# Kernel optimization log

Hardware: AMD Instinct MI355X
Metric: run time of the kernel (lower is better)

Reference implementation:

```python
import jax, jax.numpy as jnp
import numpy as np

N, E, H = 50000, 500000, 4
DIN, DH, DO, TD = 135, 128, 64, 9

def _ln(x, g, b):
    mu = jnp.mean(x, axis=-1, keepdims=True)
    v = jnp.var(x, axis=-1, keepdims=True)
    return (x - mu) / jnp.sqrt(v + 1e-5) * g + b

def _gat(x, src, dst, W, a_src, a_dst, b, n, heads, c):
    h = (x @ W).reshape(n, heads, c)                      # [N,H,C]
    es = jnp.sum(h * a_src, -1)                           # [N,H]
    ed = jnp.sum(h * a_dst, -1)
    e = jax.nn.leaky_relu(es[src] + ed[dst], 0.2)         # [E,H]
    m = jax.ops.segment_max(e, dst, num_segments=n)       # segment softmax over dst
    ex = jnp.exp(e - m[dst])
    den = jax.ops.segment_sum(ex, dst, num_segments=n)
    alpha = ex / (den[dst] + 1e-16)
    out = jax.ops.segment_sum(h[src] * alpha[..., None], dst, num_segments=n)
    return jnp.mean(out, axis=1) + b                      # concat=False -> head mean

def setup_inputs() -> dict:
    key = jax.random.key(0)
    ks = jax.random.split(key, 32)
    rn = lambda i, shape: jax.random.normal(ks[i], shape, jnp.float32) * 0.05
    inp = {}
    inp['x'] = jax.random.normal(ks[0], (N, DIN), jnp.float32)
    inp['edge_index'] = jax.random.randint(ks[1], (2, E), 0, N, jnp.int32)
    inp['edge_attr'] = jnp.ones((E, 1), jnp.float32)
    inp['W_in'] = rn(2, (DIN, DH)); inp['b_in'] = jnp.zeros((DH,), jnp.float32)
    inp['g1W'] = rn(3, (DH, H * DH)); inp['g1as'] = rn(4, (H, DH)); inp['g1ad'] = rn(5, (H, DH)); inp['g1b'] = jnp.zeros((DH,), jnp.float32)
    inp['g2W'] = rn(6, (DH, H * DH)); inp['g2as'] = rn(7, (H, DH)); inp['g2ad'] = rn(8, (H, DH)); inp['g2b'] = jnp.zeros((DH,), jnp.float32)
    inp['g3W'] = rn(9, (DH, H * DO)); inp['g3as'] = rn(10, (H, DO)); inp['g3ad'] = rn(11, (H, DO)); inp['g3b'] = jnp.zeros((DO,), jnp.float32)
    inp['r1W'] = rn(12, (DH, DH)); inp['r1b'] = jnp.zeros((DH,), jnp.float32)
    inp['r2W'] = rn(13, (DH, DH)); inp['r2b'] = jnp.zeros((DH,), jnp.float32)
    inp['r3W'] = rn(14, (DH, DO)); inp['r3b'] = jnp.zeros((DO,), jnp.float32)
    inp['n1g'] = jnp.ones((DH,), jnp.float32); inp['n1b'] = jnp.zeros((DH,), jnp.float32)
    inp['n2g'] = jnp.ones((DH,), jnp.float32); inp['n2b'] = jnp.zeros((DH,), jnp.float32)
    inp['n3g'] = jnp.ones((DO,), jnp.float32); inp['n3b'] = jnp.zeros((DO,), jnp.float32)
    inp['tw'] = jnp.float32(0.3)
    inp['c1W'] = rn(15, (DO, DO)); inp['c1b'] = jnp.zeros((DO,), jnp.float32)
    inp['clg'] = jnp.ones((DO,), jnp.float32); inp['clb'] = jnp.zeros((DO,), jnp.float32)
    inp['c2W'] = rn(16, (DO, 2)); inp['c2b'] = jnp.zeros((2,), jnp.float32)
    return inp

def reference(x, edge_index, edge_attr, W_in, b_in, g1W, g1as, g1ad, g1b,
              g2W, g2as, g2ad, g2b, g3W, g3as, g3ad, g3b,
              r1W, r1b, r2W, r2b, r3W, r3b,
              n1g, n1b, n2g, n2b, n3g, n3b, tw,
              c1W, c1b, clg, clb, c2W, c2b):
    n = x.shape[0]
    src0, dst0 = edge_index[0], edge_index[1]
    loop = jnp.arange(n, dtype=edge_index.dtype)          # GATConv add_self_loops=True
    src = jnp.concatenate([src0, loop])
    dst = jnp.concatenate([dst0, loop])
    # vectorized temporal cosine similarity over original edges
    t = x[:, -TD:]
    ti, tj = t[src0], t[dst0]
    nrm = jnp.maximum(jnp.linalg.norm(ti, axis=-1), 1e-8) * jnp.maximum(jnp.linalg.norm(tj, axis=-1), 1e-8)
    sim = jnp.sum(ti * tj, -1) / nrm
    scale = 1.0 + 0.1 * jnp.mean(1.0 + tw * sim)
    h = x @ W_in + b_in
    id1 = h
    h = _gat(h, src, dst, g1W, g1as, g1ad, g1b, n, H, DH) * scale
    h = _ln(jax.nn.relu(h) + id1 @ r1W + r1b, n1g, n1b)
    id2 = h
    h = _gat(h, src, dst, g2W, g2as, g2ad, g2b, n, H, DH) * scale
    h = _ln(jax.nn.relu(h) + id2 @ r2W + r2b, n2g, n2b)
    id3 = h
    h = _gat(h, src, dst, g3W, g3as, g3ad, g3b, n, H, DO)
    h = _ln(jax.nn.relu(h) + id3 @ r3W + r3b, n3g, n3b)
    ego = h[0:1]
    z = jax.nn.relu(ego @ c1W + c1b)
    z = _ln(z, clg, clb)
    return z @ c2W + c2b
```

## Files before the change

kernel.cpp:

```cpp
#include <hip/hip_runtime.h>

#define AGENT __HIP_MEMORY_SCOPE_AGENT

constexpr int TD = 9, TDP = 12, DIN = 135;
constexpr int CAPD = 64;
constexpr int CAP3 = 256, CAP2 = 1024, CAP1 = 4096;
constexpr int NBM = 512;
constexpr int LSTRIDE = 32;
constexpr int NGRP = 16;
constexpr int GSZ = NBM / NGRP;
constexpr int NSET = 8;
constexpr int NLINE = 64;
constexpr int PB = 8;

struct P {
  const float* x; const int* src; const int* dst; int N; int E;
  const float *W_in,*b_in,*g1W,*g1as,*g1ad,*g1b,*g2W,*g2as,*g2ad,*g2b,*g3W,*g3as,*g3ad,*g3b;
  const float *r1W,*r1b,*r2W,*r2b,*r3W,*r3b,*n1g,*n1b,*n2g,*n2b,*n3g,*n3b;
  const float *tw,*c1W,*c1b,*clg,*clb,*c2W,*c2b;
  float* tp;
  int *deg, *bk;
  int *m3,*m2,*m1,*list3,*list2,*list1,*cnts;
  int *barc,*barr,*barg;
  float *h0,*hh1,*es1,*ed1,*h1,*hh2,*es2,*ed2,*h2,*hh3,*es3,*ed3,*h3;
  float* dout;
};

__device__ __forceinline__ float lrelu(float v) { return v >= 0.f ? v : 0.2f * v; }

__device__ __forceinline__ void stg(float* pp, float v) { __hip_atomic_store(pp, v, __ATOMIC_RELAXED, AGENT); }
__device__ __forceinline__ void stg(int* pp, int v)   { __hip_atomic_store(pp, v, __ATOMIC_RELAXED, AGENT); }

__device__ __forceinline__ void claim_node(int v, int* __restrict__ m, int* __restrict__ list,
                                           int* __restrict__ cnt, int cap) {
  if (atomicCAS(&m[v], -1, -2) == -1) {
    int pos = atomicAdd(cnt, 1);
    if (pos < cap) { stg(&list[pos], v); stg(&m[v], pos); } else { stg(&m[v], -3); }
  }
}

__device__ __forceinline__ void mid_barrier(const P& p, int& lgen, int* amroot_s) {
  __syncthreads();
  int g = lgen + 1;
  if (threadIdx.x == 0) {
    *amroot_s = 0;
    int* gc = &p.barc[(((g & (NSET - 1)) * NGRP) + (blockIdx.x & (NGRP - 1))) * LSTRIDE];
    if (__hip_atomic_fetch_add(gc, 1, __ATOMIC_RELAXED, AGENT) == GSZ - 1) {
      int* rc = &p.barr[(g & (NSET - 1)) * LSTRIDE];
      if (__hip_atomic_fetch_add(rc, 1, __ATOMIC_RELAXED, AGENT) == NGRP - 1) *amroot_s = 1;
    }
  }
  __syncthreads();
  if (*amroot_s) {
    if (threadIdx.x < NLINE)
      __hip_atomic_store(&p.barg[threadIdx.x * LSTRIDE], g, __ATOMIC_RELAXED, AGENT);
  } else if (threadIdx.x == 0) {
    int* line = &p.barg[(blockIdx.x & (NLINE - 1)) * LSTRIDE];
    while (__hip_atomic_load(line, __ATOMIC_RELAXED, AGENT) < g)
      __builtin_amdgcn_s_sleep(8);
  }
  __syncthreads();
  lgen = g;
}

__global__ void k_prep(P p) {
  int gt = blockIdx.x * blockDim.x + threadIdx.x;
  int GT = gridDim.x * blockDim.x;
  int n3 = 3 * p.N;
  int4* mv = (int4*)p.m3;
  int4 neg = make_int4(-1, -1, -1, -1);
  int nv = n3 >> 2;
  for (int i = gt; i < nv; i += GT) mv[i] = neg;
  for (int i = (nv << 2) + gt; i < n3; i += GT) p.m3[i] = -1;
  int4* dv = (int4*)p.deg;
  int4 z4 = make_int4(0, 0, 0, 0);
  int ndv = p.N >> 2;
  for (int i = gt; i < ndv; i += GT) dv[i] = z4;
  for (int i = (ndv << 2) + gt; i < p.N; i += GT) p.deg[i] = 0;
  if (gt < 64) p.cnts[gt] = 0;
  for (int i = gt; i < NSET * NGRP * LSTRIDE; i += GT) p.barc[i] = 0;
  for (int i = gt; i < NSET * LSTRIDE; i += GT) p.barr[i] = 0;
  for (int i = gt; i < NLINE * LSTRIDE; i += GT) p.barg[i] = 0;
  int total = p.N * TDP;
  for (int i = gt; i < total; i += GT) {
    int v = i / TDP, k = i - v * TDP;
    p.tp[i] = (k < TD) ? p.x[(size_t)v * DIN + (DIN - TD) + k] : 0.f;
  }
}

__global__ void k_scan(P p) {
  __shared__ float wred[4];
  int tid = threadIdx.x;
  int gt = blockIdx.x * blockDim.x + tid, GT = gridDim.x * blockDim.x;
  if (gt == 0) claim_node(0, p.m3, p.list3, &p.cnts[0], CAP3);
  const float4* t4 = (const float4*)p.tp;
  float local = 0.f;
  auto edge_proc = [&](int s, int d) {
    int slot = atomicAdd(&p.deg[d], 1);
    if (slot < CAPD) p.bk[(size_t)d * CAPD + slot] = s;
    if (d == 0) claim_node(s, p.m3, p.list3, &p.cnts[0], CAP3);
    float4 a0 = t4[s * 3], a1 = t4[s * 3 + 1], a2 = t4[s * 3 + 2];
    float4 b0 = t4[d * 3], b1 = t4[d * 3 + 1], b2 = t4[d * 3 + 2];
    float dot = a0.x*b0.x + a0.y*b0.y + a0.z*b0.z + a0.w*b0.w
              + a1.x*b1.x + a1.y*b1.y + a1.z*b1.z + a1.w*b1.w
              + a2.x*b2.x;
    float na = a0.x*a0.x + a0.y*a0.y + a0.z*a0.z + a0.w*a0.w
             + a1.x*a1.x + a1.y*a1.y + a1.z*a1.z + a1.w*a1.w
             + a2.x*a2.x;
    float nb = b0.x*b0.x + b0.y*b0.y + b0.z*b0.z + b0.w*b0.w
             + b1.x*b1.x + b1.y*b1.y + b1.z*b1.z + b1.w*b1.w
             + b2.x*b2.x;
    local += dot / (fmaxf(sqrtf(na), 1e-8f) * fmaxf(sqrtf(nb), 1e-8f));
  };
  int nq4 = p.E >> 2;
  const int4* s4p = (const int4*)p.src;
  const int4* d4p = (const int4*)p.dst;
  for (int q = gt; q < nq4; q += GT) {
    int4 s4 = s4p[q], d4 = d4p[q];
    edge_proc(s4.x, d4.x); edge_proc(s4.y, d4.y); edge_proc(s4.z, d4.z); edge_proc(s4.w, d4.w);
  }
  for (int e = (nq4 << 2) + gt; e < p.E; e += GT) edge_proc(p.src[e], p.dst[e]);
  for (int off = 32; off > 0; off >>= 1) local += __shfl_down(local, off, 64);
  if ((tid & 63) == 0) wred[tid >> 6] = local;
  __syncthreads();
  if (tid == 0) atomicAdd((float*)&p.cnts[8], wred[0] + wred[1] + wred[2] + wred[3]);
}

template <int C, int ONEXT>
__device__ void gat_dev(const P& p, int nq, const int* lst, const int* mPrev,
                        const float* hh, const float* es, const float* ed, const float* hres,
                        const float* gb, const float* rW, const float* rb,
                        const float* ng, const float* nbv, float scale,
                        float* hout, const float* Wn, const float* avn, const float* bvn,
                        float* hhn, float* esn, float* edn,
                        float* elog, int* eposs, float* ev_s, float* sh,
                        float* hres_s, float* shln, float* psn, float* pdn, float* sc2) {
  const int Wd = 4 * C, R = Wd / 256;
  int tid = threadIdx.x;
  for (int q = blockIdx.x; q < nq; q += gridDim.x) {
    int v = lst[q];
    int sp = mPrev[v];
    int nb = min(p.deg[v], CAPD);
    for (int j = tid; j < nb; j += 256) {
      int pu = mPrev[p.bk[(size_t)v * CAPD + j]];
      eposs[j] = pu;
      const float* ep = &es[(size_t)pu * 4];
      elog[0 * CAPD + j] = ep[0]; elog[1 * CAPD + j] = ep[1];
      elog[2 * CAPD + j] = ep[2]; elog[3 * CAPD + j] = ep[3];
    }
    if (tid < 4) { ev_s[tid] = es[(size_t)sp * 4 + tid]; ev_s[4 + tid] = ed[(size_t)sp * 4 + tid]; }
    for (int k = tid; k < 128; k += 256) hres_s[k] = hres[(size_t)sp * 128 + k];
    __syncthreads();
#pragma unroll
    for (int r = 0; r < R; r++) {
      int w = r * 256 + tid, a = w / C;
      float edv = ev_s[4 + a];
      float eself = lrelu(ev_s[a] + edv);
      float mx = eself;
      for (int j = 0; j < nb; j++) mx = fmaxf(mx, lrelu(elog[a * CAPD + j] + edv));
      float den = __expf(eself - mx);
      for (int j = 0; j < nb; j++) den += __expf(lrelu(elog[a * CAPD + j] + edv) - mx);
      float rden = 1.f / (den + 1e-16f);
      float s = __expf(eself - mx) * rden * hh[(size_t)sp * Wd + w];
      for (int j = 0; j < nb; j++)
        s += __expf(lrelu(elog[a * CAPD + j] + edv) - mx) * rden * hh[(size_t)eposs[j] * Wd + w];
      sh[w] = s;
    }
    __syncthreads();
    float val = 0.f;
    if (tid < C) {
      float g = 0.25f * (sh[tid] + sh[C + tid] + sh[2 * C + tid] + sh[3 * C + tid]) + gb[tid];
      g *= scale;
      g = fmaxf(g, 0.f);
      float rr = rb[tid];
      for (int k = 0; k < 128; k++) rr += hres_s[k] * rW[(size_t)k * C + tid];
      val = g + rr;
      shln[tid] = val;
    }
    __syncthreads();
    if (tid == 0) {
      float s1 = 0.f, s2 = 0.f;
      for (int k = 0; k < C; k++) { float u = shln[k]; s1 += u; s2 += u * u; }
      float mu = s1 / (float)C;
      sc2[0] = mu;
      sc2[1] = rsqrtf(fmaxf(s2 / (float)C - mu * mu, 0.f) + 1e-5f);
    }
    __syncthreads();
    if (tid < C) {
      float o = (val - sc2[0]) * sc2[1] * ng[tid] + nbv[tid];
      stg(&hout[(size_t)q * C + tid], o);
      shln[tid] = o;
    }
    __syncthreads();
    if (ONEXT > 0) {
      for (int j = tid; j < ONEXT; j += 256) {
        float a2 = 0.f;
        for (int k = 0; k < C; k++) a2 += shln[k] * Wn[(size_t)k * ONEXT + j];
        stg(&hhn[(size_t)q * ONEXT + j], a2);
        psn[j] = a2 * avn[j]; pdn[j] = a2 * bvn[j];
      }
      __syncthreads();
      if (tid < 8) {
        const int CN = ONEXT / 4; int a = tid & 3;
        const float* pr = (tid < 4) ? psn : pdn;
        float s = 0.f;
        for (int cc = 0; cc < CN; cc++) s += pr[a * CN + cc];
        stg(&(tid < 4 ? esn : edn)[(size_t)q * 4 + a], s);
      }
      __syncthreads();
    }
  }
}

__global__ __launch_bounds__(256, 2) void k_mid(P p) {
  __shared__ float xs8[PB][DIN];
  __shared__ float hs8[PB][128];
  __shared__ float psn[512], pdn[512];
  __shared__ int   vid8[PB];
  __shared__ float elog[4 * CAPD];
  __shared__ int   eposs[CAPD];
  __shared__ float ev_s[8], sc2[2];
  __shared__ float sh[512], hres_s[128], shln[128];
  __shared__ float zcl[64];
  __shared__ int   amroot_s;

  int tid = threadIdx.x, bid = blockIdx.x;
  int lgen = 0;
  float scale = 1.1f + 0.1f * p.tw[0] *
      __int_as_float(__hip_atomic_load(&p.cnts[8], __ATOMIC_RELAXED, AGENT)) / (float)p.E;

  {
    int c3 = min(__hip_atomic_load(&p.cnts[0], __ATOMIC_RELAXED, AGENT), CAP3);
    for (int q = bid; q < c3; q += NBM) {
      int v = p.list3[q];
      if (tid == 0) claim_node(v, p.m2, p.list2, &p.cnts[1], CAP2);
      int nb = min(p.deg[v], CAPD);
      for (int j = tid; j < nb; j += 256)
        claim_node(p.bk[(size_t)v * CAPD + j], p.m2, p.list2, &p.cnts[1], CAP2);
    }
  }
  mid_barrier(p, lgen, &amroot_s);

  {
    int c2 = min(__hip_atomic_load(&p.cnts[1], __ATOMIC_RELAXED, AGENT), CAP2);
    for (int q = bid; q < c2; q += NBM) {
      int v = p.list2[q];
      if (tid == 0) claim_node(v, p.m1, p.list1, &p.cnts[2], CAP1);
      int nb = min(p.deg[v], CAPD);
      for (int j = tid; j < nb; j += 256)
        claim_node(p.bk[(size_t)v * CAPD + j], p.m1, p.list1, &p.cnts[2], CAP1);
    }
  }
  mid_barrier(p, lgen, &amroot_s);

  {
    int c1 = min(__hip_atomic_load(&p.cnts[2], __ATOMIC_RELAXED, AGENT), CAP1);
    int ngp = (c1 + PB - 1) / PB;
    for (int g = bid; g < ngp; g += NBM) {
      int base = g * PB, nn = min(PB, c1 - base);
      if (tid < nn) vid8[tid] = p.list1[base + tid];
      __syncthreads();
      for (int idx = tid; idx < nn * DIN; idx += 256) {
        int u = idx / DIN, k = idx - u * DIN;
        xs8[u][k] = p.x[(size_t)vid8[u] * DIN + k];
      }
      __syncthreads();
      if (tid < 128) {
        float a[PB]; float bi = p.b_in[tid];
#pragma unroll
        for (int u = 0; u < PB; u++) a[u] = bi;
        for (int k = 0; k < DIN; k++) {
          float w = p.W_in[(size_t)k * 128 + tid];
#pragma unroll
          for (int u = 0; u < PB; u++) a[u] += xs8[u][k] * w;
        }
#pragma unroll
        for (int u = 0; u < PB; u++) {
          hs8[u][tid] = a[u];
          if (u < nn) stg(&p.h0[(size_t)(base + u) * 128 + tid], a[u]);
        }
      }
      __syncthreads();
      float bsv[2][PB];
#pragma unroll
      for (int jj = 0; jj < 2; jj++) {
        int j = jj * 256 + tid;
        float b[PB];
#pragma unroll
        for (int u = 0; u < PB; u++) b[u] = 0.f;
        for (int k = 0; k < 128; k++) {
          float w = p.g1W[(size_t)k * 512 + j];
#pragma unroll
          for (int u = 0; u < PB; u++) b[u] += hs8[u][k] * w;
        }
#pragma unroll
        for (int u = 0; u < PB; u++) {
          bsv[jj][u] = b[u];
          if (u < nn) stg(&p.hh1[(size_t)(base + u) * 512 + j], b[u]);
        }
      }
      for (int u = 0; u < nn; u++) {
#pragma unroll
        for (int jj = 0; jj < 2; jj++) {
          int j = jj * 256 + tid;
          psn[j] = bsv[jj][u] * p.g1as[j];
          pdn[j] = bsv[jj][u] * p.g1ad[j];
        }
        __syncthreads();
        if (tid < 8) {
          int a = tid & 3;
          const float* pr = (tid < 4) ? psn : pdn;
          float s = 0.f;
          for (int cc = 0; cc < 128; cc++) s += pr[a * 128 + cc];
          stg(&(tid < 4 ? p.es1 : p.ed1)[(size_t)(base + u) * 4 + a], s);
        }
        __syncthreads();
      }
    }
  }
  mid_barrier(p, lgen, &amroot_s);

  {
    int c2 = min(__hip_atomic_load(&p.cnts[1], __ATOMIC_RELAXED, AGENT), CAP2);
    gat_dev<128, 512>(p, c2, p.list2, p.m1, p.hh1, p.es1, p.ed1, p.h0,
                      p.g1b, p.r1W, p.r1b, p.n1g, p.n1b, scale,
                      p.h1, p.g2W, p.g2as, p.g2ad, p.hh2, p.es2, p.ed2,
                      elog, eposs, ev_s, sh, hres_s, shln, psn, pdn, sc2);
  }
  mid_barrier(p, lgen, &amroot_s);

  {
    int c3 = min(__hip_atomic_load(&p.cnts[0], __ATOMIC_RELAXED, AGENT), CAP3);
    gat_dev<128, 256>(p, c3, p.list3, p.m2, p.hh2, p.es2, p.ed2, p.h1,
                      p.g2b, p.r2W, p.r2b, p.n2g, p.n2b, scale,
                      p.h2, p.g3W, p.g3as, p.g3ad, p.hh3, p.es3, p.ed3,
                      elog, eposs, ev_s, sh, hres_s, shln, psn, pdn, sc2);
  }
  mid_barrier(p, lgen, &amroot_s);

  if (bid == 0) {
    int zero = 0;
    gat_dev<64, 0>(p, 1, &zero , p.m3,
                   p.hh3, p.es3, p.ed3, p.h2,
                   p.g3b, p.r3W, p.r3b, p.n3g, p.n3b, 1.f,
                   p.h3, nullptr, nullptr, nullptr, nullptr, nullptr, nullptr,
                   elog, eposs, ev_s, sh, hres_s, shln, psn, pdn, sc2);
    if (tid < 64) {
      float az = p.c1b[tid];
      for (int k = 0; k < 64; k++) az += shln[k] * p.c1W[k * 64 + tid];
      zcl[tid] = fmaxf(az, 0.f);
    }
    __syncthreads();
    if (tid == 0) {
      float s1 = 0.f, s2 = 0.f;
      for (int k = 0; k < 64; k++) { float u = zcl[k]; s1 += u; s2 += u * u; }
      float mu = s1 / 64.f;
      float rstd = rsqrtf(fmaxf(s2 / 64.f - mu * mu, 0.f) + 1e-5f);
      float o0 = p.c2b[0], o1 = p.c2b[1];
      for (int k = 0; k < 64; k++) {
        float zn = (zcl[k] - mu) * rstd * p.clg[k] + p.clb[k];
        o0 += zn * p.c2W[k * 2 + 0];
        o1 += zn * p.c2W[k * 2 + 1];
      }
      p.dout[0] = o0; p.dout[1] = o1;
    }
  }
}

extern "C" void kernel_launch(void* const* d_in, const int* in_sizes, int n_in,
                              void* d_out, int out_size, void* d_ws, size_t ws_size,
                              hipStream_t stream) {
  P p;
  p.x = (const float*)d_in[0];
  const int* ei = (const int*)d_in[1];
  p.N = in_sizes[0] / DIN;
  p.E = in_sizes[1] / 2;
  p.src = ei; p.dst = ei + p.E;
  p.W_in = (const float*)d_in[3]; p.b_in = (const float*)d_in[4];
  p.g1W = (const float*)d_in[5]; p.g1as = (const float*)d_in[6]; p.g1ad = (const float*)d_in[7]; p.g1b = (const float*)d_in[8];
  p.g2W = (const float*)d_in[9]; p.g2as = (const float*)d_in[10]; p.g2ad = (const float*)d_in[11]; p.g2b = (const float*)d_in[12];
  p.g3W = (const float*)d_in[13]; p.g3as = (const float*)d_in[14]; p.g3ad = (const float*)d_in[15]; p.g3b = (const float*)d_in[16];
  p.r1W = (const float*)d_in[17]; p.r1b = (const float*)d_in[18];
  p.r2W = (const float*)d_in[19]; p.r2b = (const float*)d_in[20];
  p.r3W = (const float*)d_in[21]; p.r3b = (const float*)d_in[22];
  p.n1g = (const float*)d_in[23]; p.n1b = (const float*)d_in[24];
  p.n2g = (const float*)d_in[25]; p.n2b = (const float*)d_in[26];
  p.n3g = (const float*)d_in[27]; p.n3b = (const float*)d_in[28];
  p.tw  = (const float*)d_in[29];
  p.c1W = (const float*)d_in[30]; p.c1b = (const float*)d_in[31];
  p.clg = (const float*)d_in[32]; p.clb = (const float*)d_in[33];
  p.c2W = (const float*)d_in[34]; p.c2b = (const float*)d_in[35];
  p.dout = (float*)d_out;

  char* B = (char*)d_ws;
  size_t off = 0;
  auto take = [&](size_t nbytes) -> char* {
    char* r = B + off;
    off += (nbytes + 255) & ~(size_t)255;
    return r;
  };
  p.cnts  = (int*)take(256);
  p.barc  = (int*)take((size_t)NSET * NGRP * LSTRIDE * 4);
  p.barr  = (int*)take((size_t)NSET * LSTRIDE * 4);
  p.barg  = (int*)take((size_t)NLINE * LSTRIDE * 4);
  p.m3    = (int*)take((size_t)3 * p.N * 4);
  p.m2 = p.m3 + p.N; p.m1 = p.m2 + p.N;
  p.tp    = (float*)take((size_t)p.N * TDP * 4);
  p.deg   = (int*)take((size_t)p.N * 4);
  p.bk    = (int*)take((size_t)p.N * CAPD * 4);
  p.list3 = (int*)take(CAP3 * 4);
  p.list2 = (int*)take(CAP2 * 4);
  p.list1 = (int*)take(CAP1 * 4);
  p.h0    = (float*)take((size_t)CAP1 * 128 * 4);
  p.hh1   = (float*)take((size_t)CAP1 * 512 * 4);
  p.es1   = (float*)take((size_t)CAP1 * 16);
  p.ed1   = (float*)take((size_t)CAP1 * 16);
  p.h1    = (float*)take((size_t)CAP2 * 128 * 4);
  p.hh2   = (float*)take((size_t)CAP2 * 512 * 4);
  p.es2   = (float*)take((size_t)CAP2 * 16);
  p.ed2   = (float*)take((size_t)CAP2 * 16);
  p.h2    = (float*)take((size_t)CAP3 * 128 * 4);
  p.hh3   = (float*)take((size_t)CAP3 * 256 * 4);
  p.es3   = (float*)take((size_t)CAP3 * 16);
  p.ed3   = (float*)take((size_t)CAP3 * 16);
  p.h3    = (float*)take(64 * 4);

  k_prep<<<1024, 256, 0, stream>>>(p);
  k_scan<<<1024, 256, 0, stream>>>(p);
  k_mid<<<NBM, 256, 0, stream>>>(p);
}
```

Measured before the change: 134.9 us.

## Replace grid barriers with per-item dataflow flags and merge frontier expansion passes

Four grid-wide barriers in the persistent mid kernel are replaced with fine-grained ready flags. Each layer's producer group or node sets a flag, and consumers spin only on the flags of the neighbours they read. The 2-hop and 3-hop frontier claims are merged into a single pass by expanding newly claimed nodes in place, which removes one barrier. This lets work from successive layers overlap across blocks. The cost is spin-wait traffic and a risk of deadlock or ordering problems, since flags use relaxed atomics and spinners assume producers are resident.

```diff
diff --git a/kernel.cpp b/kernel.cpp
--- a/kernel.cpp
+++ b/kernel.cpp
@@ -7,11 +7,11 @@
 constexpr int CAP3 = 256, CAP2 = 1024, CAP1 = 4096;
 constexpr int NBM = 512;
 constexpr int LSTRIDE = 32;
-constexpr int NGRP = 16;
-constexpr int GSZ = NBM / NGRP;
+constexpr int NGRP = 16, GSZ = NBM / NGRP;
 constexpr int NSET = 8;
 constexpr int NLINE = 64;
 constexpr int PB = 8;
+constexpr int NGC = CAP1 / PB;
 
 struct P {
   const float* x; const int* src; const int* dst; int N; int E;
@@ -22,6 +22,7 @@
   int *deg, *bk;
   int *m3,*m2,*m1,*list3,*list2,*list1,*cnts;
   int *barc,*barr,*barg;
+  int *fc,*fd,*fe;
   float *h0,*hh1,*es1,*ed1,*h1,*hh2,*es2,*ed2,*h2,*hh3,*es3,*ed3,*h3;
   float* dout;
 };
@@ -31,12 +32,18 @@
 __device__ __forceinline__ void stg(float* pp, float v) { __hip_atomic_store(pp, v, __ATOMIC_RELAXED, AGENT); }
 __device__ __forceinline__ void stg(int* pp, int v)   { __hip_atomic_store(pp, v, __ATOMIC_RELAXED, AGENT); }
 
-__device__ __forceinline__ void claim_node(int v, int* __restrict__ m, int* __restrict__ list,
+__device__ __forceinline__ void spinf(const int* f) {
+  while (__hip_atomic_load((int*)f, __ATOMIC_RELAXED, AGENT) == 0) __builtin_amdgcn_s_sleep(2);
+}
+
+__device__ __forceinline__ bool claim_node(int v, int* __restrict__ m, int* __restrict__ list,
                                            int* __restrict__ cnt, int cap) {
   if (atomicCAS(&m[v], -1, -2) == -1) {
     int pos = atomicAdd(cnt, 1);
     if (pos < cap) { stg(&list[pos], v); stg(&m[v], pos); } else { stg(&m[v], -3); }
-  }
+    return true;
+  }
+  return false;
 }
 
 __device__ __forceinline__ void mid_barrier(const P& p, int& lgen, int* amroot_s) {
@@ -81,6 +88,9 @@
   for (int i = gt; i < NSET * NGRP * LSTRIDE; i += GT) p.barc[i] = 0;
   for (int i = gt; i < NSET * LSTRIDE; i += GT) p.barr[i] = 0;
   for (int i = gt; i < NLINE * LSTRIDE; i += GT) p.barg[i] = 0;
+  for (int i = gt; i < NGC; i += GT) p.fc[i] = 0;
+  for (int i = gt; i < CAP2; i += GT) p.fd[i] = 0;
+  for (int i = gt; i < CAP3; i += GT) p.fe[i] = 0;
   int total = p.N * TDP;
   for (int i = gt; i < total; i += GT) {
     int v = i / TDP, k = i - v * TDP;
@@ -126,90 +136,96 @@
   if (tid == 0) atomicAdd((float*)&p.cnts[8], wred[0] + wred[1] + wred[2] + wred[3]);
 }
 
-template <int C, int ONEXT>
-__device__ void gat_dev(const P& p, int nq, const int* lst, const int* mPrev,
-                        const float* hh, const float* es, const float* ed, const float* hres,
-                        const float* gb, const float* rW, const float* rb,
-                        const float* ng, const float* nbv, float scale,
-                        float* hout, const float* Wn, const float* avn, const float* bvn,
-                        float* hhn, float* esn, float* edn,
-                        float* elog, int* eposs, float* ev_s, float* sh,
-                        float* hres_s, float* shln, float* psn, float* pdn, float* sc2) {
+template <int C, int ONEXT, int FDIV>
+__device__ void gat_flag(const P& p, int q, const int* lst, const int* mPrev,
+                         const int* flagIn, int* flagOut,
+                         const float* hh, const float* es, const float* ed, const float* hres,
+                         const float* gb, const float* rW, const float* rb,
+                         const float* ng, const float* nbv, float scale,
+                         float* hout, const float* Wn, const float* avn, const float* bvn,
+                         float* hhn, float* esn, float* edn,
+                         float* elog, int* eposs, float* ev_s, float* sh,
+                         float* hres_s, float* shln, float* psn, float* pdn, float* sc2) {
   const int Wd = 4 * C, R = Wd / 256;
   int tid = threadIdx.x;
-  for (int q = blockIdx.x; q < nq; q += gridDim.x) {
-    int v = lst[q];
-    int sp = mPrev[v];
-    int nb = min(p.deg[v], CAPD);
-    for (int j = tid; j < nb; j += 256) {
-      int pu = mPrev[p.bk[(size_t)v * CAPD + j]];
-      eposs[j] = pu;
-      const float* ep = &es[(size_t)pu * 4];
-      elog[0 * CAPD + j] = ep[0]; elog[1 * CAPD + j] = ep[1];
-      elog[2 * CAPD + j] = ep[2]; elog[3 * CAPD + j] = ep[3];
-    }
-    if (tid < 4) { ev_s[tid] = es[(size_t)sp * 4 + tid]; ev_s[4 + tid] = ed[(size_t)sp * 4 + tid]; }
-    for (int k = tid; k < 128; k += 256) hres_s[k] = hres[(size_t)sp * 128 + k];
+  int v = lst[q];
+  int sp = mPrev[v];
+  int nb = min(p.deg[v], CAPD);
+  if (tid == 0) spinf(&flagIn[max(sp, 0) / FDIV]);
+  for (int j = tid; j < nb; j += 256) {
+    int pu = mPrev[p.bk[(size_t)v * CAPD + j]];
+    eposs[j] = pu;
+    spinf(&flagIn[max(pu, 0) / FDIV]);
+  }
+  __syncthreads();
+  for (int j = tid; j < nb; j += 256) {
+    int pu = eposs[j];
+    const float* ep = &es[(size_t)pu * 4];
+    elog[0 * CAPD + j] = ep[0]; elog[1 * CAPD + j] = ep[1];
+    elog[2 * CAPD + j] = ep[2]; elog[3 * CAPD + j] = ep[3];
+  }
+  if (tid < 4) { ev_s[tid] = es[(size_t)sp * 4 + tid]; ev_s[4 + tid] = ed[(size_t)sp * 4 + tid]; }
+  for (int k = tid; k < 128; k += 256) hres_s[k] = hres[(size_t)sp * 128 + k];
+  __syncthreads();
+#pragma unroll
+  for (int r = 0; r < R; r++) {
+    int w = r * 256 + tid, a = w / C;
+    float edv = ev_s[4 + a];
+    float eself = lrelu(ev_s[a] + edv);
+    float mx = eself;
+    for (int j = 0; j < nb; j++) mx = fmaxf(mx, lrelu(elog[a * CAPD + j] + edv));
+    float den = __expf(eself - mx);
+    for (int j = 0; j < nb; j++) den += __expf(lrelu(elog[a * CAPD + j] + edv) - mx);
+    float rden = 1.f / (den + 1e-16f);
+    float s = __expf(eself - mx) * rden * hh[(size_t)sp * Wd + w];
+    for (int j = 0; j < nb; j++)
+      s += __expf(lrelu(elog[a * CAPD + j] + edv) - mx) * rden * hh[(size_t)eposs[j] * Wd + w];
+    sh[w] = s;
+  }
+  __syncthreads();
+  float val = 0.f;
+  if (tid < C) {
+    float g = 0.25f * (sh[tid] + sh[C + tid] + sh[2 * C + tid] + sh[3 * C + tid]) + gb[tid];
+    g *= scale;
+    g = fmaxf(g, 0.f);
+    float rr = rb[tid];
+    for (int k = 0; k < 128; k++) rr += hres_s[k] * rW[(size_t)k * C + tid];
+    val = g + rr;
+    shln[tid] = val;
+  }
+  __syncthreads();
+  if (tid == 0) {
+    float s1 = 0.f, s2 = 0.f;
+    for (int k = 0; k < C; k++) { float u = shln[k]; s1 += u; s2 += u * u; }
+    float mu = s1 / (float)C;
+    sc2[0] = mu;
+    sc2[1] = rsqrtf(fmaxf(s2 / (float)C - mu * mu, 0.f) + 1e-5f);
+  }
+  __syncthreads();
+  if (tid < C) {
+    float o = (val - sc2[0]) * sc2[1] * ng[tid] + nbv[tid];
+    stg(&hout[(size_t)q * C + tid], o);
+    shln[tid] = o;
+  }
+  __syncthreads();
+  if (ONEXT > 0) {
+    for (int j = tid; j < ONEXT; j += 256) {
+      float a2 = 0.f;
+      for (int k = 0; k < C; k++) a2 += shln[k] * Wn[(size_t)k * ONEXT + j];
+      stg(&hhn[(size_t)q * ONEXT + j], a2);
+      psn[j] = a2 * avn[j]; pdn[j] = a2 * bvn[j];
+    }
     __syncthreads();
-#pragma unroll
-    for (int r = 0; r < R; r++) {
-      int w = r * 256 + tid, a = w / C;
-      float edv = ev_s[4 + a];
-      float eself = lrelu(ev_s[a] + edv);
-      float mx = eself;
-      for (int j = 0; j < nb; j++) mx = fmaxf(mx, lrelu(elog[a * CAPD + j] + edv));
-      float den = __expf(eself - mx);
-      for (int j = 0; j < nb; j++) den += __expf(lrelu(elog[a * CAPD + j] + edv) - mx);
-      float rden = 1.f / (den + 1e-16f);
-      float s = __expf(eself - mx) * rden * hh[(size_t)sp * Wd + w];
-      for (int j = 0; j < nb; j++)
-        s += __expf(lrelu(elog[a * CAPD + j] + edv) - mx) * rden * hh[(size_t)eposs[j] * Wd + w];
-      sh[w] = s;
-    }
-    __syncthreads();
-    float val = 0.f;
-    if (tid < C) {
-      float g = 0.25f * (sh[tid] + sh[C + tid] + sh[2 * C + tid] + sh[3 * C + tid]) + gb[tid];
-      g *= scale;
-      g = fmaxf(g, 0.f);
-      float rr = rb[tid];
-      for (int k = 0; k < 128; k++) rr += hres_s[k] * rW[(size_t)k * C + tid];
-      val = g + rr;
-      shln[tid] = val;
-    }
-    __syncthreads();
-    if (tid == 0) {
-      float s1 = 0.f, s2 = 0.f;
-      for (int k = 0; k < C; k++) { float u = shln[k]; s1 += u; s2 += u * u; }
-      float mu = s1 / (float)C;
-      sc2[0] = mu;
-      sc2[1] = rsqrtf(fmaxf(s2 / (float)C - mu * mu, 0.f) + 1e-5f);
-    }
-    __syncthreads();
-    if (tid < C) {
-      float o = (val - sc2[0]) * sc2[1] * ng[tid] + nbv[tid];
-      stg(&hout[(size_t)q * C + tid], o);
-      shln[tid] = o;
-    }
-    __syncthreads();
-    if (ONEXT > 0) {
-      for (int j = tid; j < ONEXT; j += 256) {
-        float a2 = 0.f;
-        for (int k = 0; k < C; k++) a2 += shln[k] * Wn[(size_t)k * ONEXT + j];
-        stg(&hhn[(size_t)q * ONEXT + j], a2);
-        psn[j] = a2 * avn[j]; pdn[j] = a2 * bvn[j];
-      }
-      __syncthreads();
-      if (tid < 8) {
-        const int CN = ONEXT / 4; int a = tid & 3;
-        const float* pr = (tid < 4) ? psn : pdn;
-        float s = 0.f;
-        for (int cc = 0; cc < CN; cc++) s += pr[a * CN + cc];
-        stg(&(tid < 4 ? esn : edn)[(size_t)q * 4 + a], s);
-      }
-      __syncthreads();
-    }
-  }
+    if (tid < 8) {
+      const int CN = ONEXT / 4; int a = tid & 3;
+      const float* pr = (tid < 4) ? psn : pdn;
+      float s = 0.f;
+      for (int cc = 0; cc < CN; cc++) s += pr[a * CN + cc];
+      stg(&(tid < 4 ? esn : edn)[(size_t)q * 4 + a], s);
+    }
+  }
+  __syncthreads();
+  if (tid == 0 && flagOut) stg(&flagOut[q], 1);
 }
 
 __global__ __launch_bounds__(256, 2) void k_mid(P p) {
@@ -223,6 +239,7 @@
   __shared__ float sh[512], hres_s[128], shln[128];
   __shared__ float zcl[64];
   __shared__ int   amroot_s;
+  __shared__ int   shw;
 
   int tid = threadIdx.x, bid = blockIdx.x;
   int lgen = 0;
@@ -233,28 +250,33 @@
     int c3 = min(__hip_atomic_load(&p.cnts[0], __ATOMIC_RELAXED, AGENT), CAP3);
     for (int q = bid; q < c3; q += NBM) {
       int v = p.list3[q];
-      if (tid == 0) claim_node(v, p.m2, p.list2, &p.cnts[1], CAP2);
+      if (tid == 0) shw = claim_node(v, p.m2, p.list2, &p.cnts[1], CAP2) ? 1 : 0;
+      __syncthreads();
       int nb = min(p.deg[v], CAPD);
-      for (int j = tid; j < nb; j += 256)
-        claim_node(p.bk[(size_t)v * CAPD + j], p.m2, p.list2, &p.cnts[1], CAP2);
+      for (int j = tid; j < nb; j += 256) {
+        int u = p.bk[(size_t)v * CAPD + j];
+        if (claim_node(u, p.m2, p.list2, &p.cnts[1], CAP2)) {
+          claim_node(u, p.m1, p.list1, &p.cnts[2], CAP1);
+          int nbu = min(p.deg[u], CAPD);
+          for (int k2 = 0; k2 < nbu; k2++)
+            claim_node(p.bk[(size_t)u * CAPD + k2], p.m1, p.list1, &p.cnts[2], CAP1);
+        }
+      }
+      if (shw) {
+        if (tid == 0) claim_node(v, p.m1, p.list1, &p.cnts[2], CAP1);
+        for (int j = tid; j < nb; j += 256)
+          claim_node(p.bk[(size_t)v * CAPD + j], p.m1, p.list1, &p.cnts[2], CAP1);
+      }
+      __syncthreads();
     }
   }
   mid_barrier(p, lgen, &amroot_s);
 
+  int c1 = min(__hip_atomic_load(&p.cnts[2], __ATOMIC_RELAXED, AGENT), CAP1);
+  int c2 = min(__hip_atomic_load(&p.cnts[1], __ATOMIC_RELAXED, AGENT), CAP2);
+  int c3 = min(__hip_atomic_load(&p.cnts[0], __ATOMIC_RELAXED, AGENT), CAP3);
+
   {
-    int c2 = min(__hip_atomic_load(&p.cnts[1], __ATOMIC_RELAXED, AGENT), CAP2);
-    for (int q = bid; q < c2; q += NBM) {
-      int v = p.list2[q];
-      if (tid == 0) claim_node(v, p.m1, p.list1, &p.cnts[2], CAP1);
-      int nb = min(p.deg[v], CAPD);
-      for (int j = tid; j < nb; j += 256)
-        claim_node(p.bk[(size_t)v * CAPD + j], p.m1, p.list1, &p.cnts[2], CAP1);
-    }
-  }
-  mid_barrier(p, lgen, &amroot_s);
-
-  {
-    int c1 = min(__hip_atomic_load(&p.cnts[2], __ATOMIC_RELAXED, AGENT), CAP1);
     int ngp = (c1 + PB - 1) / PB;
     for (int g = bid; g < ngp; g += NBM) {
       int base = g * PB, nn = min(PB, c1 - base);
@@ -316,35 +338,31 @@
         }
         __syncthreads();
       }
-    }
-  }
-  mid_barrier(p, lgen, &amroot_s);
-
-  {
-    int c2 = min(__hip_atomic_load(&p.cnts[1], __ATOMIC_RELAXED, AGENT), CAP2);
-    gat_dev<128, 512>(p, c2, p.list2, p.m1, p.hh1, p.es1, p.ed1, p.h0,
-                      p.g1b, p.r1W, p.r1b, p.n1g, p.n1b, scale,
-                      p.h1, p.g2W, p.g2as, p.g2ad, p.hh2, p.es2, p.ed2,
-                      elog, eposs, ev_s, sh, hres_s, shln, psn, pdn, sc2);
-  }
-  mid_barrier(p, lgen, &amroot_s);
-
-  {
-    int c3 = min(__hip_atomic_load(&p.cnts[0], __ATOMIC_RELAXED, AGENT), CAP3);
-    gat_dev<128, 256>(p, c3, p.list3, p.m2, p.hh2, p.es2, p.ed2, p.h1,
-                      p.g2b, p.r2W, p.r2b, p.n2g, p.n2b, scale,
-                      p.h2, p.g3W, p.g3as, p.g3ad, p.hh3, p.es3, p.ed3,
-                      elog, eposs, ev_s, sh, hres_s, shln, psn, pdn, sc2);
-  }
-  mid_barrier(p, lgen, &amroot_s);
+      if (tid == 0) stg(&p.fc[g], 1);
+    }
+  }
+
+  for (int q = bid; q < c2; q += NBM)
+    gat_flag<128, 512, PB>(p, q, p.list2, p.m1, p.fc, p.fd,
+                           p.hh1, p.es1, p.ed1, p.h0,
+                           p.g1b, p.r1W, p.r1b, p.n1g, p.n1b, scale,
+                           p.h1, p.g2W, p.g2as, p.g2ad, p.hh2, p.es2, p.ed2,
+                           elog, eposs, ev_s, sh, hres_s, shln, psn, pdn, sc2);
+
+  for (int q = bid; q < c3; q += NBM)
+    gat_flag<128, 256, 1>(p, q, p.list3, p.m2, p.fd, p.fe,
+                          p.hh2, p.es2, p.ed2, p.h1,
+                          p.g2b, p.r2W, p.r2b, p.n2g, p.n2b, scale,
+                          p.h2, p.g3W, p.g3as, p.g3ad, p.hh3, p.es3, p.ed3,
+                          elog, eposs, ev_s, sh, hres_s, shln, psn, pdn, sc2);
 
   if (bid == 0) {
     int zero = 0;
-    gat_dev<64, 0>(p, 1, &zero , p.m3,
-                   p.hh3, p.es3, p.ed3, p.h2,
-                   p.g3b, p.r3W, p.r3b, p.n3g, p.n3b, 1.f,
-                   p.h3, nullptr, nullptr, nullptr, nullptr, nullptr, nullptr,
-                   elog, eposs, ev_s, sh, hres_s, shln, psn, pdn, sc2);
+    gat_flag<64, 0, 1>(p, 0, &zero, p.m3, p.fe, nullptr,
+                       p.hh3, p.es3, p.ed3, p.h2,
+                       p.g3b, p.r3W, p.r3b, p.n3g, p.n3b, 1.f,
+                       p.h3, nullptr, nullptr, nullptr, nullptr, nullptr, nullptr,
+                       elog, eposs, ev_s, sh, hres_s, shln, psn, pdn, sc2);
     if (tid < 64) {
       float az = p.c1b[tid];
       for (int k = 0; k < 64; k++) az += shln[k] * p.c1W[k * 64 + tid];
@@ -403,6 +421,9 @@
   p.barc  = (int*)take((size_t)NSET * NGRP * LSTRIDE * 4);
   p.barr  = (int*)take((size_t)NSET * LSTRIDE * 4);
   p.barg  = (int*)take((size_t)NLINE * LSTRIDE * 4);
+  p.fc    = (int*)take(NGC * 4);
+  p.fd    = (int*)take(CAP2 * 4);
+  p.fe    = (int*)take(CAP3 * 4);
   p.m3    = (int*)take((size_t)3 * p.N * 4);
   p.m2 = p.m3 + p.N; p.m1 = p.m2 + p.N;
   p.tp    = (float*)take((size_t)p.N * TDP * 4);
```

Measured after the change: 143.8 us. 1.07x slower.
